# Kernel optimization log

Hardware: AMD Instinct MI355X
Metric: run time of the kernel (lower is better)

## Reference

```python
import jax, jax.numpy as jnp
import numpy as np

B, C, S, F = 128, 5, 512, 3
U = 256          # encoder units
RU = 2 * U       # decoder units / bidirectional encoder width


def _lstm_cell(x_t, h, c, Wk, Wr, b):
    # Keras LSTM gate order: i, f, g(cell), o
    z = x_t @ Wk + h @ Wr + b
    i, f, g, o = jnp.split(z, 4, axis=-1)
    c_new = jax.nn.sigmoid(f) * c + jax.nn.sigmoid(i) * jnp.tanh(g)
    h_new = jax.nn.sigmoid(o) * jnp.tanh(c_new)
    return h_new, c_new


def _masked_lstm(xs, mask, Wk, Wr, b, units):
    # xs: [B,S,D], mask: [B,S] bool. Keras semantics: masked steps carry
    # previous state and previous output (== previous h for LSTM).
    Bn = xs.shape[0]

    def step(carry, inp):
        h, c = carry
        x_t, m_t = inp
        h_n, c_n = _lstm_cell(x_t, h, c, Wk, Wr, b)
        m = m_t[:, None]
        h2 = jnp.where(m, h_n, h)
        c2 = jnp.where(m, c_n, c)
        return (h2, c2), h2

    init = (jnp.zeros((Bn, units), xs.dtype), jnp.zeros((Bn, units), xs.dtype))
    _, outs = jax.lax.scan(step, init, (jnp.swapaxes(xs, 0, 1), mask.T))
    return jnp.swapaxes(outs, 0, 1)  # [B,S,units]


def setup_inputs() -> dict:
    key = jax.random.key(0)
    k = jax.random.split(key, 10)
    s = 0.05
    rn = lambda kk, sh: jax.random.normal(kk, sh, jnp.float32) * s
    return {
        "x": jax.random.normal(k[0], (B, C, S, F), jnp.float32),
        "Wf_k": rn(k[1], (C, 4 * U)), "Wf_r": rn(k[2], (U, 4 * U)), "bf": jnp.zeros((4 * U,), jnp.float32),
        "Wb_k": rn(k[3], (C, 4 * U)), "Wb_r": rn(k[4], (U, 4 * U)), "bb": jnp.zeros((4 * U,), jnp.float32),
        "Wd_k": rn(k[5], (C, 4 * RU)), "Wd_r": rn(k[6], (RU, 4 * RU)), "bd": jnp.zeros((4 * RU,), jnp.float32),
        "W_attn": rn(k[7], (RU + C, 1)), "b_attn": jnp.zeros((1,), jnp.float32),
        "W_dense": rn(k[8], (RU + RU, C)), "b_dense": jnp.zeros((C,), jnp.float32),
    }


def reference(x, Wf_k, Wf_r, bf, Wb_k, Wb_r, bb, Wd_k, Wd_r, bd,
              W_attn, b_attn, W_dense, b_dense):
    xt = jnp.transpose(x, (0, 2, 1, 3))          # [B,S,C,F]
    mask = xt[:, :, 0, 2] != 0                   # tf.cast(..., bool)
    xs = xt[:, :, :, 0]                          # [B,S,C]

    fwd = _masked_lstm(xs, mask, Wf_k, Wf_r, bf, U)
    bwd = _masked_lstm(xs[:, ::-1], mask[:, ::-1], Wb_k, Wb_r, bb, U)[:, ::-1]
    enc = jnp.concatenate([fwd, bwd], axis=-1)   # [B,S,RU]

    # attention(concat([tile(x_t), enc])) is linear -> split the weight:
    Wx, We = W_attn[:C, 0], W_attn[C:, 0]
    enc_scores = jnp.einsum('bsd,d->bs', enc, We) + b_attn[0]  # [B,S]

    hidden0 = enc[:, -1, :]                      # [B,RU]
    x0 = xs[:, 0, :]                             # [B,C]

    def dec_step(carry, _):
        hidden, x_t = carry
        scores = enc_scores + (x_t @ Wx)[:, None]             # [B,S]
        alpha = jax.nn.softmax(scores, axis=1)
        attn = jnp.einsum('bs,bsd->bd', alpha, enc)           # [B,RU]
        # decoder LSTM on a single timestep, initial_state=[hidden, attn]
        h_new, _c = _lstm_cell(x_t, hidden, attn, Wd_k, Wd_r, bd)
        x_new = jnp.concatenate([h_new, attn], axis=-1) @ W_dense + b_dense
        return (h_new, x_new), x_new

    _, ys = jax.lax.scan(dec_step, (hidden0, x0), None, length=S - 1)  # [S-1,B,C]
    return jnp.transpose(ys, (1, 2, 0))[..., None]           # [B,C,S-1,1]
```

## Files before the change

### kernel.cpp

```cpp
#include <hip/hip_runtime.h>
#include <math.h>

#define BATCH 128
#define CCH 5
#define SEQ 512
#define UNITS 256
#define RU 512

#define ENC_N 33554432

__device__ __forceinline__ float sigmoidf_(float v) {
    return 1.0f / (1.0f + __expf(-v));
}
__device__ __forceinline__ float tanhf_(float v) {
    float e = __expf(2.0f * v);
    return 1.0f - 2.0f / (e + 1.0f);
}
__device__ __forceinline__ void astoreu64(unsigned long long* p, unsigned long long v) {
    __hip_atomic_store(p, v, __ATOMIC_RELAXED, __HIP_MEMORY_SCOPE_AGENT);
}
__device__ __forceinline__ unsigned long long aloadu64(const unsigned long long* p) {
    return __hip_atomic_load(p, __ATOMIC_RELAXED, __HIP_MEMORY_SCOPE_AGENT);
}
__device__ __forceinline__ unsigned long long packht(unsigned tag, float h) {
    return ((unsigned long long)tag << 32) | (unsigned long long)__float_as_uint(h);
}

__global__ __attribute__((amdgpu_flat_work_group_size(1024, 1024),
                          amdgpu_waves_per_eu(4, 4)))
void encoder_kernel(const float* __restrict__ x,
                    const float* __restrict__ Wf_k, const float* __restrict__ Wf_r,
                    const float* __restrict__ bf,
                    const float* __restrict__ Wb_k, const float* __restrict__ Wb_r,
                    const float* __restrict__ bb,
                    float* __restrict__ enc, unsigned long long* __restrict__ hx)
{
    const int bid  = blockIdx.x;
    const int dir  = bid >> 7;
    const int tile = (bid >> 3) & 15;
    const int jsl  = bid & 7;
    const int bg0  = tile * 8;
    const float* __restrict__ Wk   = dir ? Wb_k : Wf_k;
    const float* __restrict__ Wr   = dir ? Wb_r : Wf_r;
    const float* __restrict__ bias = dir ? bb : bf;
    const int tid = threadIdx.x;
    const int wv  = tid >> 6;
    const int l   = tid & 63;
    const int g0 = ((l >> 5) << 8) + jsl * 32 + (l & 31);

    __shared__ float zp[16][8][128];
    __shared__ float __align__(16) hLe[2][8][260];
    __shared__ float zred[8][128];
    __shared__ float WkL[5][128];
    __shared__ float biasL[128];
    __shared__ unsigned char mL[8][SEQ];
    __shared__ float xLe[2][8][8];

    for (int i = tid; i < 2 * 8 * 260; i += 1024) ((float*)hLe)[i] = 0.0f;
    if (tid < 128) biasL[tid] = bias[((tid >> 5) << 8) + jsl * 32 + (tid & 31)];
    if (tid >= 128 && tid < 768) {
        int i = tid - 128, c = i >> 7, cl = i & 127;
        WkL[c][cl] = Wk[c * 1024 + ((cl >> 5) << 8) + jsl * 32 + (cl & 31)];
    }
    for (int i = tid; i < 8 * SEQ; i += 1024) {
        int b = i >> 9, tt = i & (SEQ - 1);
        mL[b][tt] = (x[((size_t)((bg0 + b) * CCH) * SEQ + tt) * 3 + 2] != 0.0f) ? 1 : 0;
    }
    float wr0[16], wr1[16];
    {
        const float* wbase = Wr + (size_t)(wv * 16) * 1024 + g0;
        #pragma unroll
        for (int r = 0; r < 16; ++r) {
            wr0[r] = wbase[(size_t)r * 1024];
            wr1[r] = wbase[(size_t)r * 1024 + 512];
        }
        #pragma unroll
        for (int r = 0; r < 16; ++r)
            asm volatile("" : "+v"(wr0[r]), "+v"(wr1[r]));
    }
    float creg = 0.0f, hreg = 0.0f;
    __syncthreads();

    for (int t = 0; t < SEQ; ++t) {
        const int cur = t & 1;
        const int ts = dir ? (SEQ - 1 - t) : t;
        if (t > 0) {
            int b = l >> 3, u0 = wv * 16 + (l & 7) * 2;
            const unsigned long long* hp = hx
                + ((size_t)(dir * 2 + ((t - 1) & 1)) * 16 + tile) * 2048
                + b * 256 + u0;
            const unsigned tg = (unsigned)t;
            unsigned long long v0, v1;
            for (int it = 0;; ++it) {
                v0 = aloadu64(hp);
                v1 = aloadu64(hp + 1);
                if ((unsigned)(v0 >> 32) == tg && (unsigned)(v1 >> 32) == tg) break;
                if (it > (1 << 22)) break;
                __builtin_amdgcn_s_sleep(1);
            }
            hLe[cur][b][u0]     = __uint_as_float((unsigned)v0);
            hLe[cur][b][u0 + 1] = __uint_as_float((unsigned)v1);
        }
        if (tid >= 960 && tid < 1000) {
            int i = tid - 960, b = i / 5, c = i - b * 5;
            xLe[cur][b][c] = x[((size_t)((bg0 + b) * CCH + c) * SEQ + ts) * 3];
        }

        float accA[8], accB[8];
        #pragma unroll
        for (int b = 0; b < 8; ++b) {
            float a0 = 0.f, a1 = 0.f;
            const float4* hp4 = (const float4*)&hLe[cur][b][wv * 16];
            #pragma unroll
            for (int q = 0; q < 4; ++q) {
                float4 h4 = hp4[q];
                a0 = fmaf(h4.x, wr0[4*q+0], a0); a1 = fmaf(h4.x, wr1[4*q+0], a1);
                a0 = fmaf(h4.y, wr0[4*q+1], a0); a1 = fmaf(h4.y, wr1[4*q+1], a1);
                a0 = fmaf(h4.z, wr0[4*q+2], a0); a1 = fmaf(h4.z, wr1[4*q+2], a1);
                a0 = fmaf(h4.w, wr0[4*q+3], a0); a1 = fmaf(h4.w, wr1[4*q+3], a1);
            }
            accA[b] = a0; accB[b] = a1;
        }
        #pragma unroll
        for (int b = 0; b < 8; ++b) {
            zp[wv][b][l]      = accA[b];
            zp[wv][b][64 + l] = accB[b];
        }
        __syncthreads();

        {
            int b = tid >> 7, cl = tid & 127;
            float sum = biasL[cl];
            #pragma unroll
            for (int s = 0; s < 16; ++s) sum += zp[s][b][cl];
            #pragma unroll
            for (int c = 0; c < 5; ++c) sum = fmaf(xLe[cur][b][c], WkL[c][cl], sum);
            zred[b][cl] = sum;
        }
        __syncthreads();

        if (tid < 256) {
            int b = tid >> 5, u = tid & 31;
            float zi = zred[b][u];
            float zf = zred[b][32 + u];
            float zg = zred[b][64 + u];
            float zo = zred[b][96 + u];
            float cn = sigmoidf_(zf) * creg + sigmoidf_(zi) * tanhf_(zg);
            float hn = sigmoidf_(zo) * tanhf_(cn);
            int m = mL[b][ts];
            float h2 = m ? hn : hreg;
            float c2 = m ? cn : creg;
            creg = c2; hreg = h2;
            astoreu64(&hx[((size_t)(dir * 2 + cur) * 16 + tile) * 2048
                          + b * 256 + jsl * 32 + u],
                      packht((unsigned)(t + 1), h2));
            enc[((size_t)(bg0 + b) * SEQ + ts) * RU + dir * UNITS + jsl * 32 + u] = h2;
        }
    }
}

__global__ __launch_bounds__(256)
void attn_kernel(const float* __restrict__ enc,
                 const float* __restrict__ W_attn, const float* __restrict__ b_attn,
                 const float* __restrict__ W_dense, const float* __restrict__ b_dense,
                 const float* __restrict__ x,
                 float* __restrict__ attn_ws, float* __restrict__ hidden_ws,
                 float* __restrict__ xbuf, float* __restrict__ xconst)
{
    const int b = blockIdx.x;
    const int tid = threadIdx.x;
    const int lane = tid & 63;
    const int wv = tid >> 6;

    __shared__ float WeL[RU];
    __shared__ float scoresL[SEQ];
    __shared__ float red[256];
    __shared__ float attnL[RU];

    WeL[tid]       = W_attn[CCH + tid];
    WeL[tid + 256] = W_attn[CCH + tid + 256];
    __syncthreads();

    const float* __restrict__ encb = enc + (size_t)b * SEQ * RU;
    const float batt = b_attn[0];

    for (int s = wv; s < SEQ; s += 4) {
        const float* row = encb + (size_t)s * RU;
        float p = 0.0f;
        #pragma unroll
        for (int i = 0; i < 8; ++i) {
            int d = lane * 8 + i;
            p = fmaf(row[d], WeL[d], p);
        }
        #pragma unroll
        for (int o = 32; o; o >>= 1) p += __shfl_xor(p, o);
        if (lane == 0) scoresL[s] = p + batt;
    }
    __syncthreads();

    float m = fmaxf(scoresL[tid], scoresL[tid + 256]);
    red[tid] = m;
    __syncthreads();
    for (int st = 128; st; st >>= 1) {
        if (tid < st) red[tid] = fmaxf(red[tid], red[tid + st]);
        __syncthreads();
    }
    const float mx = red[0];
    __syncthreads();
    float e0 = __expf(scoresL[tid] - mx);
    float e1 = __expf(scoresL[tid + 256] - mx);
    red[tid] = e0 + e1;
    __syncthreads();
    for (int st = 128; st; st >>= 1) {
        if (tid < st) red[tid] += red[tid + st];
        __syncthreads();
    }
    const float sinv = 1.0f / red[0];
    __syncthreads();
    scoresL[tid]       = e0 * sinv;
    scoresL[tid + 256] = e1 * sinv;
    __syncthreads();

    float a0 = 0.0f, a1 = 0.0f;
    for (int s = 0; s < SEQ; ++s) {
        float al = scoresL[s];
        a0 = fmaf(al, encb[(size_t)s * RU + tid], a0);
        a1 = fmaf(al, encb[(size_t)s * RU + tid + 256], a1);
    }
    attn_ws[(size_t)b * RU + tid]       = a0;
    attn_ws[(size_t)b * RU + tid + 256] = a1;
    attnL[tid] = a0;
    attnL[tid + 256] = a1;
    hidden_ws[(size_t)b * RU + tid]       = encb[(size_t)(SEQ - 1) * RU + tid];
    hidden_ws[(size_t)b * RU + tid + 256] = encb[(size_t)(SEQ - 1) * RU + tid + 256];
    if (tid < CCH) xbuf[b * CCH + tid] = x[((size_t)(b * CCH + tid) * SEQ + 0) * 3];
    __syncthreads();

    if (tid < CCH) {
        float acc = b_dense[tid];
        for (int d = 0; d < RU; ++d)
            acc = fmaf(attnL[d], W_dense[(RU + d) * CCH + tid], acc);
        xconst[b * CCH + tid] = acc;
    }
}

__global__ __attribute__((amdgpu_flat_work_group_size(1024, 1024),
                          amdgpu_waves_per_eu(4, 4)))
void decoder_kernel(const float* __restrict__ Wd_k, const float* __restrict__ Wd_r,
                    const float* __restrict__ bd,
                    const float* __restrict__ W_dense,
                    const float* __restrict__ attn_ws, const float* __restrict__ hidden_ws,
                    const float* __restrict__ xbuf, const float* __restrict__ xconst,
                    unsigned long long* __restrict__ hx,
                    float* __restrict__ out)
{
    const int bid  = blockIdx.x;
    const int tile = bid >> 4;
    const int jsl  = bid & 15;
    const int bg0  = tile * 8;
    const int tid  = threadIdx.x;
    const int wv   = tid >> 6;
    const int l    = tid & 63;
    const int g0 = ((l >> 5) << 9) + jsl * 32 + (l & 31);

    __shared__ float zp[16][8][128];
    __shared__ float __align__(16) hL[2][8][516];
    __shared__ float zred[8][128];
    __shared__ float WdL[RU * CCH];
    __shared__ float WkL[5][128];
    __shared__ float biasL[128];
    __shared__ float xL[8][8], xcL[8][8];

    for (int i = tid; i < RU * CCH; i += 1024) WdL[i] = W_dense[i];
    if (tid < 128) biasL[tid] = bd[((tid >> 5) << 9) + jsl * 32 + (tid & 31)];
    if (tid >= 128 && tid < 768) {
        int i = tid - 128, c = i >> 7, cl = i & 127;
        WkL[c][cl] = Wd_k[c * 2048 + ((cl >> 5) << 9) + jsl * 32 + (cl & 31)];
    }
    if (tid < 64) {
        int b = tid >> 3, c = tid & 7;
        if (c < 5) {
            xL[b][c]  = xbuf[(bg0 + b) * CCH + c];
            xcL[b][c] = xconst[(bg0 + b) * CCH + c];
        }
    }
    {
        int f = tid * 4, b = f >> 9, u = f & (RU - 1);
        *(float4*)&hL[0][b][u] = *(const float4*)&hidden_ws[(size_t)(bg0 + b) * RU + u];
    }
    float attR = 0.0f;
    if (tid < 256)
        attR = attn_ws[(size_t)(bg0 + (tid >> 5)) * RU + jsl * 32 + (tid & 31)];
    float wr0[32], wr1[32];
    {
        const float* wbase = Wd_r + (size_t)(wv * 32) * 2048 + g0;
        #pragma unroll
        for (int r = 0; r < 32; ++r) {
            wr0[r] = wbase[(size_t)r * 2048];
            wr1[r] = wbase[(size_t)r * 2048 + 1024];
        }
        #pragma unroll
        for (int r = 0; r < 32; ++r)
            asm volatile("" : "+v"(wr0[r]), "+v"(wr1[r]));
    }
    __syncthreads();

    for (int t = 0; t < SEQ - 1; ++t) {
        const int cur = t & 1;
        if (t > 0) {
            int b = l >> 3, u0 = wv * 32 + (l & 7) * 4;
            const unsigned long long* hp = hx
                + ((size_t)((t - 1) & 1) * 16 + tile) * 4096 + b * 512 + u0;
            const unsigned tg = (unsigned)t;
            unsigned long long v0, v1, v2, v3;
            for (int it = 0;; ++it) {
                v0 = aloadu64(hp);     v1 = aloadu64(hp + 1);
                v2 = aloadu64(hp + 2); v3 = aloadu64(hp + 3);
                if ((unsigned)(v0 >> 32) == tg && (unsigned)(v1 >> 32) == tg &&
                    (unsigned)(v2 >> 32) == tg && (unsigned)(v3 >> 32) == tg) break;
                if (it > (1 << 22)) break;
                __builtin_amdgcn_s_sleep(1);
            }
            float4 hv;
            hv.x = __uint_as_float((unsigned)v0);
            hv.y = __uint_as_float((unsigned)v1);
            hv.z = __uint_as_float((unsigned)v2);
            hv.w = __uint_as_float((unsigned)v3);
            *(float4*)&hL[cur][b][u0] = hv;
        }

        float accA[8], accB[8];
        #pragma unroll
        for (int b = 0; b < 8; ++b) {
            float a0 = 0.f, a1 = 0.f;
            const float4* hp4 = (const float4*)&hL[cur][b][wv * 32];
            #pragma unroll
            for (int q = 0; q < 8; ++q) {
                float4 h4 = hp4[q];
                a0 = fmaf(h4.x, wr0[4*q+0], a0); a1 = fmaf(h4.x, wr1[4*q+0], a1);
                a0 = fmaf(h4.y, wr0[4*q+1], a0); a1 = fmaf(h4.y, wr1[4*q+1], a1);
                a0 = fmaf(h4.z, wr0[4*q+2], a0); a1 = fmaf(h4.z, wr1[4*q+2], a1);
                a0 = fmaf(h4.w, wr0[4*q+3], a0); a1 = fmaf(h4.w, wr1[4*q+3], a1);
            }
            accA[b] = a0; accB[b] = a1;
        }
        #pragma unroll
        for (int b = 0; b < 8; ++b) {
            zp[wv][b][l]      = accA[b];
            zp[wv][b][64 + l] = accB[b];
        }
        __syncthreads();

        if (t > 0) {
            for (int it = wv; it < 40; it += 16) {
                int bb = it / 5, c = it - bb * 5;
                float p = 0.f;
                #pragma unroll
                for (int q = 0; q < 8; ++q) {
                    int uu = l + (q << 6);
                    p = fmaf(hL[cur][bb][uu], WdL[uu * CCH + c], p);
                }
                #pragma unroll
                for (int o = 32; o; o >>= 1) p += __shfl_xor(p, o);
                if (l == 0) xL[bb][c] = p + xcL[bb][c];
            }
        }
        {
            int b = tid >> 7, cl = tid & 127;
            float sum = biasL[cl];
            #pragma unroll
            for (int s = 0; s < 16; ++s) sum += zp[s][b][cl];
            zred[b][cl] = sum;
        }
        __syncthreads();

        if (tid < 256) {
            int b = tid >> 5, u = tid & 31;
            float zi = zred[b][u];
            float zf = zred[b][32 + u];
            float zg = zred[b][64 + u];
            float zo = zred[b][96 + u];
            #pragma unroll
            for (int c = 0; c < 5; ++c) {
                float xv = xL[b][c];
                zi = fmaf(xv, WkL[c][u], zi);      zf = fmaf(xv, WkL[c][32 + u], zf);
                zg = fmaf(xv, WkL[c][64 + u], zg); zo = fmaf(xv, WkL[c][96 + u], zo);
            }
            float cn = sigmoidf_(zf) * attR + sigmoidf_(zi) * tanhf_(zg);
            float hn = sigmoidf_(zo) * tanhf_(cn);
            astoreu64(&hx[((size_t)cur * 16 + tile) * 4096 + b * 512 + jsl * 32 + u],
                      packht((unsigned)(t + 1), hn));
        }
        if (t > 0 && jsl == 0 && tid >= 256 && tid < 296) {
            int i = tid - 256, bb = i / 5, c = i - bb * 5;
            out[(size_t)((bg0 + bb) * CCH + c) * (SEQ - 1) + (t - 1)] = xL[bb][c];
        }
    }

    if (jsl == 0) {
        const int t = SEQ - 1;
        const int cur = t & 1;
        int b = l >> 3, u0 = wv * 32 + (l & 7) * 4;
        const unsigned long long* hp = hx
            + ((size_t)((t - 1) & 1) * 16 + tile) * 4096 + b * 512 + u0;
        const unsigned tg = (unsigned)t;
        unsigned long long v0, v1, v2, v3;
        for (int it = 0;; ++it) {
            v0 = aloadu64(hp);     v1 = aloadu64(hp + 1);
            v2 = aloadu64(hp + 2); v3 = aloadu64(hp + 3);
            if ((unsigned)(v0 >> 32) == tg && (unsigned)(v1 >> 32) == tg &&
                (unsigned)(v2 >> 32) == tg && (unsigned)(v3 >> 32) == tg) break;
            if (it > (1 << 22)) break;
            __builtin_amdgcn_s_sleep(1);
        }
        float4 hv;
        hv.x = __uint_as_float((unsigned)v0);
        hv.y = __uint_as_float((unsigned)v1);
        hv.z = __uint_as_float((unsigned)v2);
        hv.w = __uint_as_float((unsigned)v3);
        *(float4*)&hL[cur][b][u0] = hv;
        __syncthreads();
        for (int it = wv; it < 40; it += 16) {
            int bb = it / 5, c = it - bb * 5;
            float p = 0.f;
            #pragma unroll
            for (int q = 0; q < 8; ++q) {
                int uu = l + (q << 6);
                p = fmaf(hL[cur][bb][uu], WdL[uu * CCH + c], p);
            }
            #pragma unroll
            for (int o = 32; o; o >>= 1) p += __shfl_xor(p, o);
            if (l == 0)
                out[(size_t)((bg0 + bb) * CCH + c) * (SEQ - 1) + (t - 1)]
                    = p + xcL[bb][c];
        }
    }
}

extern "C" void kernel_launch(void* const* d_in, const int* in_sizes, int n_in,
                              void* d_out, int out_size, void* d_ws, size_t ws_size,
                              hipStream_t stream)
{
    const float* x       = (const float*)d_in[0];
    const float* Wf_k    = (const float*)d_in[1];
    const float* Wf_r    = (const float*)d_in[2];
    const float* bf      = (const float*)d_in[3];
    const float* Wb_k    = (const float*)d_in[4];
    const float* Wb_r    = (const float*)d_in[5];
    const float* bb      = (const float*)d_in[6];
    const float* Wd_k    = (const float*)d_in[7];
    const float* Wd_r    = (const float*)d_in[8];
    const float* bd      = (const float*)d_in[9];
    const float* W_attn  = (const float*)d_in[10];
    const float* b_attn  = (const float*)d_in[11];
    const float* W_dense = (const float*)d_in[12];
    const float* b_dense = (const float*)d_in[13];
    float* out = (float*)d_out;

    float* ws = (float*)d_ws;
    float* enc      = ws;
    float* attn_p   = ws + ENC_N;
    float* hidden_p = ws + ENC_N + 65536;
    float* xbuf_p   = ws + ENC_N + 131072;
    float* xconst_p = ws + ENC_N + 131712;
    unsigned long long* hx_e = (unsigned long long*)(ws + ENC_N);
    unsigned long long* hx_d = (unsigned long long*)(ws + 8192);

    hipMemsetAsync(hx_e, 0, 131072 * sizeof(unsigned long long), stream);
    encoder_kernel<<<256, 1024, 0, stream>>>(x, Wf_k, Wf_r, bf, Wb_k, Wb_r, bb,
                                             enc, hx_e);
    attn_kernel<<<BATCH, 256, 0, stream>>>(enc, W_attn, b_attn, W_dense, b_dense, x,
                                           attn_p, hidden_p, xbuf_p, xconst_p);
    hipMemsetAsync(hx_d, 0, 131072 * sizeof(unsigned long long), stream);
    decoder_kernel<<<256, 1024, 0, stream>>>(Wd_k, Wd_r, bd, W_dense,
                                             attn_p, hidden_p, xbuf_p, xconst_p,
                                             hx_d, out);
}
```

Baseline: 5.258 ms.

## Use packed FP32 FMA with batch-pair interleaved hidden state layout

Reorganizes the hidden-state exchange buffer and shared-memory copy so pairs of batch rows are interleaved per unit. The recurrent matvec in both the encoder and decoder can then use v_pk_fma_f32 to do two FMAs per instruction, which is meant to halve the VALU instruction count of the per-step inner loop. The producer store and consumer poll indices change to match the new layout. Inline asm packed FMAs limit compiler scheduling, and the strided reads in the dense projection may cause LDS bank conflicts.

```diff
diff --git a/kernel.cpp b/kernel.cpp
--- a/kernel.cpp
+++ b/kernel.cpp
@@ -9,6 +9,8 @@
 
 #define ENC_N 33554432
 
+typedef float v2f __attribute__((ext_vector_type(2)));
+
 __device__ __forceinline__ float sigmoidf_(float v) {
     return 1.0f / (1.0f + __expf(-v));
 }
@@ -25,6 +27,13 @@
 __device__ __forceinline__ unsigned long long packht(unsigned tag, float h) {
     return ((unsigned long long)tag << 32) | (unsigned long long)__float_as_uint(h);
 }
+
+#define PK_LO(ACC, H2, W2) \
+    asm("v_pk_fma_f32 %0, %1, %2, %0 op_sel:[0,0,0] op_sel_hi:[1,0,1]" \
+        : "+v"(ACC) : "v"(H2), "v"(W2))
+#define PK_HI(ACC, H2, W2) \
+    asm("v_pk_fma_f32 %0, %1, %2, %0 op_sel:[0,1,0] op_sel_hi:[1,1,1]" \
+        : "+v"(ACC) : "v"(H2), "v"(W2))
 
 __global__ __attribute__((amdgpu_flat_work_group_size(1024, 1024),
                           amdgpu_waves_per_eu(4, 4)))
@@ -49,14 +58,14 @@
     const int g0 = ((l >> 5) << 8) + jsl * 32 + (l & 31);
 
     __shared__ float zp[16][8][128];
-    __shared__ float __align__(16) hLe[2][8][260];
+    __shared__ float __align__(16) hPe[2][4][520];
     __shared__ float zred[8][128];
     __shared__ float WkL[5][128];
     __shared__ float biasL[128];
     __shared__ unsigned char mL[8][SEQ];
     __shared__ float xLe[2][8][8];
 
-    for (int i = tid; i < 2 * 8 * 260; i += 1024) ((float*)hLe)[i] = 0.0f;
+    for (int i = tid; i < 2 * 4 * 520; i += 1024) ((float*)hPe)[i] = 0.0f;
     if (tid < 128) biasL[tid] = bias[((tid >> 5) << 8) + jsl * 32 + (tid & 31)];
     if (tid >= 128 && tid < 768) {
         int i = tid - 128, c = i >> 7, cl = i & 127;
@@ -66,17 +75,14 @@
         int b = i >> 9, tt = i & (SEQ - 1);
         mL[b][tt] = (x[((size_t)((bg0 + b) * CCH) * SEQ + tt) * 3 + 2] != 0.0f) ? 1 : 0;
     }
-    float wr0[16], wr1[16];
+    v2f wp[16];
     {
         const float* wbase = Wr + (size_t)(wv * 16) * 1024 + g0;
         #pragma unroll
         for (int r = 0; r < 16; ++r) {
-            wr0[r] = wbase[(size_t)r * 1024];
-            wr1[r] = wbase[(size_t)r * 1024 + 512];
-        }
-        #pragma unroll
-        for (int r = 0; r < 16; ++r)
-            asm volatile("" : "+v"(wr0[r]), "+v"(wr1[r]));
+            v2f w; w.x = wbase[(size_t)r * 1024]; w.y = wbase[(size_t)r * 1024 + 512];
+            wp[r] = w;
+        }
     }
     float creg = 0.0f, hreg = 0.0f;
     __syncthreads();
@@ -85,10 +91,10 @@
         const int cur = t & 1;
         const int ts = dir ? (SEQ - 1 - t) : t;
         if (t > 0) {
-            int b = l >> 3, u0 = wv * 16 + (l & 7) * 2;
+            int p = l & 3, u0 = wv * 16 + (l >> 2);
             const unsigned long long* hp = hx
                 + ((size_t)(dir * 2 + ((t - 1) & 1)) * 16 + tile) * 2048
-                + b * 256 + u0;
+                + (size_t)u0 * 8 + 2 * p;
             const unsigned tg = (unsigned)t;
             unsigned long long v0, v1;
             for (int it = 0;; ++it) {
@@ -98,33 +104,39 @@
                 if (it > (1 << 22)) break;
                 __builtin_amdgcn_s_sleep(1);
             }
-            hLe[cur][b][u0]     = __uint_as_float((unsigned)v0);
-            hLe[cur][b][u0 + 1] = __uint_as_float((unsigned)v1);
+            float2 hv;
+            hv.x = __uint_as_float((unsigned)v0);
+            hv.y = __uint_as_float((unsigned)v1);
+            *(float2*)&hPe[cur][p][u0 * 2] = hv;
         }
         if (tid >= 960 && tid < 1000) {
             int i = tid - 960, b = i / 5, c = i - b * 5;
             xLe[cur][b][c] = x[((size_t)((bg0 + b) * CCH + c) * SEQ + ts) * 3];
         }
 
-        float accA[8], accB[8];
-        #pragma unroll
-        for (int b = 0; b < 8; ++b) {
-            float a0 = 0.f, a1 = 0.f;
-            const float4* hp4 = (const float4*)&hLe[cur][b][wv * 16];
-            #pragma unroll
-            for (int q = 0; q < 4; ++q) {
-                float4 h4 = hp4[q];
-                a0 = fmaf(h4.x, wr0[4*q+0], a0); a1 = fmaf(h4.x, wr1[4*q+0], a1);
-                a0 = fmaf(h4.y, wr0[4*q+1], a0); a1 = fmaf(h4.y, wr1[4*q+1], a1);
-                a0 = fmaf(h4.z, wr0[4*q+2], a0); a1 = fmaf(h4.z, wr1[4*q+2], a1);
-                a0 = fmaf(h4.w, wr0[4*q+3], a0); a1 = fmaf(h4.w, wr1[4*q+3], a1);
-            }
-            accA[b] = a0; accB[b] = a1;
-        }
-        #pragma unroll
-        for (int b = 0; b < 8; ++b) {
-            zp[wv][b][l]      = accA[b];
-            zp[wv][b][64 + l] = accB[b];
+        v2f acc0[4], acc1[4];
+        #pragma unroll
+        for (int p = 0; p < 4; ++p) { acc0[p] = (v2f){0.f,0.f}; acc1[p] = (v2f){0.f,0.f}; }
+        #pragma unroll
+        for (int q = 0; q < 8; ++q) {
+            v2f w0 = wp[2 * q], w1 = wp[2 * q + 1];
+            #pragma unroll
+            for (int p = 0; p < 4; ++p) {
+                float4 A = *(const float4*)&hPe[cur][p][(wv * 16 + 2 * q) * 2];
+                v2f h0; h0.x = A.x; h0.y = A.y;
+                v2f h1; h1.x = A.z; h1.y = A.w;
+                PK_LO(acc0[p], h0, w0);
+                PK_HI(acc1[p], h0, w0);
+                PK_LO(acc0[p], h1, w1);
+                PK_HI(acc1[p], h1, w1);
+            }
+        }
+        #pragma unroll
+        for (int p = 0; p < 4; ++p) {
+            zp[wv][2 * p][l]          = acc0[p].x;
+            zp[wv][2 * p + 1][l]      = acc0[p].y;
+            zp[wv][2 * p][64 + l]     = acc1[p].x;
+            zp[wv][2 * p + 1][64 + l] = acc1[p].y;
         }
         __syncthreads();
 
@@ -152,7 +164,7 @@
             float c2 = m ? cn : creg;
             creg = c2; hreg = h2;
             astoreu64(&hx[((size_t)(dir * 2 + cur) * 16 + tile) * 2048
-                          + b * 256 + jsl * 32 + u],
+                          + (size_t)(jsl * 32 + u) * 8 + b],
                       packht((unsigned)(t + 1), h2));
             enc[((size_t)(bg0 + b) * SEQ + ts) * RU + dir * UNITS + jsl * 32 + u] = h2;
         }
@@ -264,7 +276,7 @@
     const int g0 = ((l >> 5) << 9) + jsl * 32 + (l & 31);
 
     __shared__ float zp[16][8][128];
-    __shared__ float __align__(16) hL[2][8][516];
+    __shared__ float __align__(16) hP[2][4][1040];
     __shared__ float zred[8][128];
     __shared__ float WdL[RU * CCH];
     __shared__ float WkL[5][128];
@@ -284,38 +296,36 @@
             xcL[b][c] = xconst[(bg0 + b) * CCH + c];
         }
     }
-    {
-        int f = tid * 4, b = f >> 9, u = f & (RU - 1);
-        *(float4*)&hL[0][b][u] = *(const float4*)&hidden_ws[(size_t)(bg0 + b) * RU + u];
+    for (int e = tid; e < 4096; e += 1024) {
+        int p = e >> 10, k = e & 1023;
+        hP[0][p][k] = hidden_ws[(size_t)(bg0 + 2 * p + (k & 1)) * RU + (k >> 1)];
     }
     float attR = 0.0f;
     if (tid < 256)
         attR = attn_ws[(size_t)(bg0 + (tid >> 5)) * RU + jsl * 32 + (tid & 31)];
-    float wr0[32], wr1[32];
+    v2f wp[32];
     {
         const float* wbase = Wd_r + (size_t)(wv * 32) * 2048 + g0;
         #pragma unroll
         for (int r = 0; r < 32; ++r) {
-            wr0[r] = wbase[(size_t)r * 2048];
-            wr1[r] = wbase[(size_t)r * 2048 + 1024];
-        }
-        #pragma unroll
-        for (int r = 0; r < 32; ++r)
-            asm volatile("" : "+v"(wr0[r]), "+v"(wr1[r]));
+            v2f w; w.x = wbase[(size_t)r * 2048]; w.y = wbase[(size_t)r * 2048 + 1024];
+            wp[r] = w;
+        }
     }
     __syncthreads();
 
     for (int t = 0; t < SEQ - 1; ++t) {
         const int cur = t & 1;
         if (t > 0) {
-            int b = l >> 3, u0 = wv * 32 + (l & 7) * 4;
+            int p = l & 3, u0 = wv * 32 + (l >> 2) * 2;
             const unsigned long long* hp = hx
-                + ((size_t)((t - 1) & 1) * 16 + tile) * 4096 + b * 512 + u0;
+                + ((size_t)((t - 1) & 1) * 16 + tile) * 4096
+                + (size_t)u0 * 8 + 2 * p;
             const unsigned tg = (unsigned)t;
             unsigned long long v0, v1, v2, v3;
             for (int it = 0;; ++it) {
                 v0 = aloadu64(hp);     v1 = aloadu64(hp + 1);
-                v2 = aloadu64(hp + 2); v3 = aloadu64(hp + 3);
+                v2 = aloadu64(hp + 8); v3 = aloadu64(hp + 9);
                 if ((unsigned)(v0 >> 32) == tg && (unsigned)(v1 >> 32) == tg &&
                     (unsigned)(v2 >> 32) == tg && (unsigned)(v3 >> 32) == tg) break;
                 if (it > (1 << 22)) break;
@@ -326,39 +336,44 @@
             hv.y = __uint_as_float((unsigned)v1);
             hv.z = __uint_as_float((unsigned)v2);
             hv.w = __uint_as_float((unsigned)v3);
-            *(float4*)&hL[cur][b][u0] = hv;
-        }
-
-        float accA[8], accB[8];
-        #pragma unroll
-        for (int b = 0; b < 8; ++b) {
-            float a0 = 0.f, a1 = 0.f;
-            const float4* hp4 = (const float4*)&hL[cur][b][wv * 32];
-            #pragma unroll
-            for (int q = 0; q < 8; ++q) {
-                float4 h4 = hp4[q];
-                a0 = fmaf(h4.x, wr0[4*q+0], a0); a1 = fmaf(h4.x, wr1[4*q+0], a1);
-                a0 = fmaf(h4.y, wr0[4*q+1], a0); a1 = fmaf(h4.y, wr1[4*q+1], a1);
-                a0 = fmaf(h4.z, wr0[4*q+2], a0); a1 = fmaf(h4.z, wr1[4*q+2], a1);
-                a0 = fmaf(h4.w, wr0[4*q+3], a0); a1 = fmaf(h4.w, wr1[4*q+3], a1);
-            }
-            accA[b] = a0; accB[b] = a1;
-        }
-        #pragma unroll
-        for (int b = 0; b < 8; ++b) {
-            zp[wv][b][l]      = accA[b];
-            zp[wv][b][64 + l] = accB[b];
+            *(float4*)&hP[cur][p][u0 * 2] = hv;
+        }
+
+        v2f acc0[4], acc1[4];
+        #pragma unroll
+        for (int p = 0; p < 4; ++p) { acc0[p] = (v2f){0.f,0.f}; acc1[p] = (v2f){0.f,0.f}; }
+        #pragma unroll
+        for (int q = 0; q < 16; ++q) {
+            v2f w0 = wp[2 * q], w1 = wp[2 * q + 1];
+            #pragma unroll
+            for (int p = 0; p < 4; ++p) {
+                float4 A = *(const float4*)&hP[cur][p][(wv * 32 + 2 * q) * 2];
+                v2f h0; h0.x = A.x; h0.y = A.y;
+                v2f h1; h1.x = A.z; h1.y = A.w;
+                PK_LO(acc0[p], h0, w0);
+                PK_HI(acc1[p], h0, w0);
+                PK_LO(acc0[p], h1, w1);
+                PK_HI(acc1[p], h1, w1);
+            }
+        }
+        #pragma unroll
+        for (int p = 0; p < 4; ++p) {
+            zp[wv][2 * p][l]          = acc0[p].x;
+            zp[wv][2 * p + 1][l]      = acc0[p].y;
+            zp[wv][2 * p][64 + l]     = acc1[p].x;
+            zp[wv][2 * p + 1][64 + l] = acc1[p].y;
         }
         __syncthreads();
 
         if (t > 0) {
             for (int it = wv; it < 40; it += 16) {
                 int bb = it / 5, c = it - bb * 5;
+                const int pb = bb >> 1, jb = bb & 1;
                 float p = 0.f;
                 #pragma unroll
                 for (int q = 0; q < 8; ++q) {
                     int uu = l + (q << 6);
-                    p = fmaf(hL[cur][bb][uu], WdL[uu * CCH + c], p);
+                    p = fmaf(hP[cur][pb][uu * 2 + jb], WdL[uu * CCH + c], p);
                 }
                 #pragma unroll
                 for (int o = 32; o; o >>= 1) p += __shfl_xor(p, o);
@@ -388,7 +403,8 @@
             }
             float cn = sigmoidf_(zf) * attR + sigmoidf_(zi) * tanhf_(zg);
             float hn = sigmoidf_(zo) * tanhf_(cn);
-            astoreu64(&hx[((size_t)cur * 16 + tile) * 4096 + b * 512 + jsl * 32 + u],
+            astoreu64(&hx[((size_t)cur * 16 + tile) * 4096
+                          + (size_t)(jsl * 32 + u) * 8 + b],
                       packht((unsigned)(t + 1), hn));
         }
         if (t > 0 && jsl == 0 && tid >= 256 && tid < 296) {
@@ -400,14 +416,15 @@
     if (jsl == 0) {
         const int t = SEQ - 1;
         const int cur = t & 1;
-        int b = l >> 3, u0 = wv * 32 + (l & 7) * 4;
+        int p = l & 3, u0 = wv * 32 + (l >> 2) * 2;
         const unsigned long long* hp = hx
-            + ((size_t)((t - 1) & 1) * 16 + tile) * 4096 + b * 512 + u0;
+            + ((size_t)((t - 1) & 1) * 16 + tile) * 4096
+            + (size_t)u0 * 8 + 2 * p;
         const unsigned tg = (unsigned)t;
         unsigned long long v0, v1, v2, v3;
         for (int it = 0;; ++it) {
             v0 = aloadu64(hp);     v1 = aloadu64(hp + 1);
-            v2 = aloadu64(hp + 2); v3 = aloadu64(hp + 3);
+            v2 = aloadu64(hp + 8); v3 = aloadu64(hp + 9);
             if ((unsigned)(v0 >> 32) == tg && (unsigned)(v1 >> 32) == tg &&
                 (unsigned)(v2 >> 32) == tg && (unsigned)(v3 >> 32) == tg) break;
             if (it > (1 << 22)) break;
@@ -418,21 +435,22 @@
         hv.y = __uint_as_float((unsigned)v1);
         hv.z = __uint_as_float((unsigned)v2);
         hv.w = __uint_as_float((unsigned)v3);
-        *(float4*)&hL[cur][b][u0] = hv;
+        *(float4*)&hP[cur][p][u0 * 2] = hv;
         __syncthreads();
         for (int it = wv; it < 40; it += 16) {
             int bb = it / 5, c = it - bb * 5;
-            float p = 0.f;
+            const int pb = bb >> 1, jb = bb & 1;
+            float p2 = 0.f;
             #pragma unroll
             for (int q = 0; q < 8; ++q) {
                 int uu = l + (q << 6);
-                p = fmaf(hL[cur][bb][uu], WdL[uu * CCH + c], p);
-            }
-            #pragma unroll
-            for (int o = 32; o; o >>= 1) p += __shfl_xor(p, o);
+                p2 = fmaf(hP[cur][pb][uu * 2 + jb], WdL[uu * CCH + c], p2);
+            }
+            #pragma unroll
+            for (int o = 32; o; o >>= 1) p2 += __shfl_xor(p2, o);
             if (l == 0)
                 out[(size_t)((bg0 + bb) * CCH + c) * (SEQ - 1) + (t - 1)]
-                    = p + xcL[bb][c];
+                    = p2 + xcL[bb][c];
         }
     }
 }
```

Result: slower. 6.326 ms (+20.3%).
